# Performance work log

Measured on AMD Instinct MI355X. Metric: run time of the kernel, lower is better.

Reference implementation:

```python
import jax, jax.numpy as jnp
import numpy as np

B = 1024           # number of drug pairs (graphs per side)
ATOMS = 64         # atoms per molecule
N = B * ATOMS      # total atoms per side
H = 512            # hidden_size * number_of_molecules
FFN_H = 2048
OUT = 86           # num_tasks


def setup_inputs() -> dict:
    key = jax.random.key(0)
    ks = jax.random.split(key, 12)
    inv = 1.0 / np.sqrt(H)
    inv2 = 1.0 / np.sqrt(2 * H)
    invf = 1.0 / np.sqrt(FFN_H)
    return {
        "left_output": jax.random.normal(ks[0], (B, H), jnp.float32),
        "right_output": jax.random.normal(ks[1], (B, H), jnp.float32),
        "left_atom": jax.random.normal(ks[2], (N, H), jnp.float32),
        "right_atom": jax.random.normal(ks[3], (N, H), jnp.float32),
        "left_batch": jnp.arange(N, dtype=jnp.int32) // ATOMS,
        "right_batch": jnp.arange(N, dtype=jnp.int32) // ATOMS,
        "noise": jax.random.uniform(ks[4], (B, H), jnp.float32),
        "w_i_w": jax.random.normal(ks[5], (H, H), jnp.float32) * inv,
        "w_i_b": jnp.zeros((H,), jnp.float32),
        "prj_i_w": jax.random.normal(ks[6], (H, H), jnp.float32) * inv,
        "prj_i_b": jnp.zeros((H,), jnp.float32),
        "ffn1_w": jax.random.normal(ks[7], (2 * H, FFN_H), jnp.float32) * inv2,
        "ffn1_b": jnp.zeros((FFN_H,), jnp.float32),
        "ffn2_w": jax.random.normal(ks[8], (FFN_H, OUT), jnp.float32) * invf,
        "ffn2_b": jnp.zeros((OUT,), jnp.float32),
    }


def _seg_softmax(s, seg, num_segments):
    m = jax.ops.segment_max(s, seg, num_segments=num_segments)
    e = jnp.exp(s - m[seg])
    z = jax.ops.segment_sum(e, seg, num_segments=num_segments)
    return e / z[seg]


def reference(left_output, right_output, left_atom, right_atom,
              left_batch, right_batch, noise,
              w_i_w, w_i_b, prj_i_w, prj_i_b,
              ffn1_w, ffn1_b, ffn2_w, ffn2_b):
    # repeat_interleave(left_output, degree(right_batch)) == gather by segment id
    left_align = left_output[right_batch]    # [N_r, H]
    right_align = right_output[left_batch]   # [N_l, H]

    # cross-molecule coattention scores (elementwise product + reduce)
    left_scores = jnp.sum((left_atom @ w_i_w + w_i_b) * (right_align @ prj_i_w + prj_i_b), axis=-1)
    left_scores = _seg_softmax(left_scores, left_batch, B)
    right_scores = jnp.sum((right_atom @ w_i_w + w_i_b) * (left_align @ prj_i_w + prj_i_b), axis=-1)
    right_scores = _seg_softmax(right_scores, right_batch, B)

    # attention-weighted global add pool
    h_output = jax.ops.segment_sum(left_atom * right_align * left_scores[:, None], left_batch, num_segments=B)
    t_output = jax.ops.segment_sum(right_atom * left_align * right_scores[:, None], right_batch, num_segments=B)

    # sign-directed noise perturbation (same noise for both sides, as in original)
    nrm = jnp.maximum(jnp.linalg.norm(noise, axis=-1, keepdims=True), 1e-12)
    noise_n = noise / nrm
    h_pert = h_output + jnp.sign(h_output) * noise_n * 0.1
    t_pert = t_output + jnp.sign(t_output) * noise_n * 0.1

    pair = jnp.concatenate([h_pert, t_pert], axis=-1)  # [B, 2H]
    hid = jax.nn.relu(pair @ ffn1_w + ffn1_b)
    output = hid @ ffn2_w + ffn2_b  # training mode: raw logits, no sigmoid
    return (output, h_output, h_pert, left_scores, right_scores, left_output, right_output)
```

## Files before the change

kernel.cpp:

```cpp
#include <hip/hip_runtime.h>
#include <hip/hip_bf16.h>
#include <float.h>

#define B_ 1024
#define H_ 512
#define N_ (B_ * 64)
#define FFN_ 2048
#define OUT_ 86

typedef __bf16 bf16_t;
typedef __attribute__((ext_vector_type(8))) __bf16 bf16x8;
typedef __attribute__((ext_vector_type(4))) float f32x4;

__device__ __forceinline__ float wred_sum(float v) {
#pragma unroll
  for (int m = 32; m; m >>= 1) v += __shfl_xor(v, m);
  return v;
}
__device__ __forceinline__ float wred_max(float v) {
#pragma unroll
  for (int m = 32; m; m >>= 1) v = fmaxf(v, __shfl_xor(v, m));
  return v;
}

__device__ __forceinline__ void gload_lds16(const void* g, void* l) {
  __builtin_amdgcn_global_load_lds((const __attribute__((address_space(1))) unsigned int*)g,
                                   (__attribute__((address_space(3))) unsigned int*)l, 16, 0, 0);
}

template <bool BT, bool BIAS>
__global__ __launch_bounds__(256) void gemm64(const float* __restrict__ A1, const float* __restrict__ A2,
                                              int M1, const float* __restrict__ Bm,
                                              const float* __restrict__ bias, float* __restrict__ C,
                                              int N, int K) {
  __shared__ float As[16][68];
  __shared__ float Bs[16][68];
  const int bm = blockIdx.x * 64, bn = blockIdx.y * 64;
  const float* __restrict__ A = (bm < M1) ? (A1 + (size_t)bm * K) : (A2 + (size_t)(bm - M1) * K);
  const int t = threadIdx.x;
  const int tx = t & 15, ty = t >> 4;
  float acc[4][4] = {};
  for (int k0 = 0; k0 < K; k0 += 16) {
#pragma unroll
    for (int i = 0; i < 4; i++) {
      int m = (t >> 4) + i * 16;
      As[t & 15][m] = A[(size_t)m * K + k0 + (t & 15)];
    }
    if (BT) {
#pragma unroll
      for (int i = 0; i < 4; i++) {
        int n = (t >> 4) + i * 16;
        Bs[t & 15][n] = Bm[(size_t)(bn + n) * K + k0 + (t & 15)];
      }
    } else {
#pragma unroll
      for (int i = 0; i < 4; i++) {
        int kk = (t >> 6) + i * 4;
        Bs[kk][t & 63] = Bm[(size_t)(k0 + kk) * N + bn + (t & 63)];
      }
    }
    __syncthreads();
#pragma unroll
    for (int kk = 0; kk < 16; kk++) {
      float4 av = *(const float4*)&As[kk][ty * 4];
      float4 bv = *(const float4*)&Bs[kk][tx * 4];
      float a_[4] = {av.x, av.y, av.z, av.w};
      float b_[4] = {bv.x, bv.y, bv.z, bv.w};
#pragma unroll
      for (int i = 0; i < 4; i++)
#pragma unroll
        for (int j = 0; j < 4; j++) acc[i][j] += a_[i] * b_[j];
    }
    __syncthreads();
  }
#pragma unroll
  for (int i = 0; i < 4; i++) {
    int m = bm + ty * 4 + i;
    float tmp[4];
#pragma unroll
    for (int j = 0; j < 4; j++) {
      float x = acc[i][j];
      if (BIAS) x += bias[bn + tx * 4 + j];
      tmp[j] = x;
    }
    float4 v;
    v.x = tmp[0]; v.y = tmp[1]; v.z = tmp[2]; v.w = tmp[3];
    *(float4*)&C[(size_t)m * N + bn + tx * 4] = v;
  }
}

__global__ __launch_bounds__(512, 4) void k_atoms11(const float* __restrict__ atomL, const float* __restrict__ atomR,
                                                    const float* __restrict__ uLR,
                                                    float* __restrict__ scoresL, float* __restrict__ scoresR,
                                                    float* __restrict__ pL, float* __restrict__ pR) {
  const int pair = blockIdx.x;
  const int side = pair >> 10, b = pair & 1023;
  const int t = threadIdx.x, wave = t >> 6, lane = t & 63;

  __shared__ float s_all[64];
  __shared__ float s_nrm[64];
  __shared__ float pp[8][512];

  const float* __restrict__ atom = side ? atomR : atomL;
  const float* __restrict__ u = uLR + (size_t)pair * H_;
  f32x4 u0 = *(const f32x4*)&u[lane * 4];
  f32x4 u1 = *(const f32x4*)&u[256 + lane * 4];

  const float* __restrict__ base = atom + ((size_t)b * 64 + wave * 8) * H_ + lane * 4;

  f32x4 A0[8], A1[8];
#pragma unroll
  for (int i = 0; i < 8; i++) {
    const float* r0 = base + (size_t)i * H_;
    asm volatile("global_load_dwordx4 %0, %1, off" : "=&v"(A0[i]) : "v"(r0) : "memory");
    asm volatile("global_load_dwordx4 %0, %1, off" : "=&v"(A1[i]) : "v"(r0 + 256) : "memory");
  }

  float d[8];
#pragma unroll
  for (int i = 0; i < 8; i++) {
    switch (14 - 2 * i) {
      case 14: asm volatile("s_waitcnt vmcnt(14)" ::: "memory"); break;
      case 12: asm volatile("s_waitcnt vmcnt(12)" ::: "memory"); break;
      case 10: asm volatile("s_waitcnt vmcnt(10)" ::: "memory"); break;
      case 8:  asm volatile("s_waitcnt vmcnt(8)"  ::: "memory"); break;
      case 6:  asm volatile("s_waitcnt vmcnt(6)"  ::: "memory"); break;
      case 4:  asm volatile("s_waitcnt vmcnt(4)"  ::: "memory"); break;
      case 2:  asm volatile("s_waitcnt vmcnt(2)"  ::: "memory"); break;
      default: asm volatile("s_waitcnt vmcnt(0)"  ::: "memory"); break;
    }
    __builtin_amdgcn_sched_barrier(0);
    d[i] = A0[i].x * u0.x + A0[i].y * u0.y + A0[i].z * u0.z + A0[i].w * u0.w +
           A1[i].x * u1.x + A1[i].y * u1.y + A1[i].z * u1.z + A1[i].w * u1.w;
  }

#pragma unroll
  for (int i = 0; i < 8; i++) d[i] = wred_sum(d[i]);
  if (lane < 8) {
    float myv = 0.f;
#pragma unroll
    for (int i = 0; i < 8; i++) myv = (lane == i) ? d[i] : myv;
    s_all[wave * 8 + lane] = myv;
  }
  __syncthreads();
  {
    float sv = s_all[lane];
    float M = wred_max(sv);
    float e = __expf(sv - M);
    float Z = wred_sum(e);
    float w_n = e / Z;
    if (wave == 0) {
      s_nrm[lane] = w_n;
      (side ? scoresR : scoresL)[(size_t)b * 64 + lane] = w_n;
    }
  }
  __syncthreads();

  f32x4 q0 = {0.f, 0.f, 0.f, 0.f}, q1 = {0.f, 0.f, 0.f, 0.f};
#pragma unroll
  for (int i = 0; i < 8; i++) {
    const float w = s_nrm[wave * 8 + i];
    q0.x += w * A0[i].x; q0.y += w * A0[i].y; q0.z += w * A0[i].z; q0.w += w * A0[i].w;
    q1.x += w * A1[i].x; q1.y += w * A1[i].y; q1.z += w * A1[i].z; q1.w += w * A1[i].w;
  }
  *(f32x4*)&pp[wave][lane * 4] = q0;
  *(f32x4*)&pp[wave][256 + lane * 4] = q1;
  __syncthreads();

  float v = pp[0][t] + pp[1][t] + pp[2][t] + pp[3][t] +
            pp[4][t] + pp[5][t] + pp[6][t] + pp[7][t];
  (side ? pR : pL)[(size_t)b * H_ + t] = v;
}

__global__ __launch_bounds__(512) void k_pert(const float* __restrict__ lo, const float* __restrict__ ro,
                                              const float* __restrict__ noise,
                                              const float* __restrict__ pL, const float* __restrict__ pR,
                                              float* __restrict__ h_out, float* __restrict__ h_pert,
                                              bf16_t* __restrict__ pairbf) {
  const int b = blockIdx.x, t = threadIdx.x;
  float nv = noise[(size_t)b * H_ + t];
  float sq = nv * nv;
  sq = wred_sum(sq);
  __shared__ float red[8];
  if ((t & 63) == 0) red[t >> 6] = sq;
  __syncthreads();
  float tot = 0.f;
#pragma unroll
  for (int i = 0; i < 8; i++) tot += red[i];
  float nrm = fmaxf(sqrtf(tot), 1e-12f);
  float nn = nv / nrm * 0.1f;
  float h = ro[(size_t)b * H_ + t] * pL[(size_t)b * H_ + t];
  float tt = lo[(size_t)b * H_ + t] * pR[(size_t)b * H_ + t];
  float sh = (h > 0.f) ? 1.f : ((h < 0.f) ? -1.f : 0.f);
  float st = (tt > 0.f) ? 1.f : ((tt < 0.f) ? -1.f : 0.f);
  float hp = h + sh * nn;
  float tp = tt + st * nn;
  h_out[(size_t)b * H_ + t] = h;
  h_pert[(size_t)b * H_ + t] = hp;
  pairbf[(size_t)b * 1024 + t] = (bf16_t)hp;
  pairbf[(size_t)b * 1024 + 512 + t] = (bf16_t)tp;
}

__global__ __launch_bounds__(256) void k_w1t(const float* __restrict__ W1, bf16_t* __restrict__ W1t) {
  __shared__ float tile[32][33];
  const int bx = blockIdx.x;
  const int by = blockIdx.y;
  const int tx = threadIdx.x & 31, ty = threadIdx.x >> 5;
#pragma unroll
  for (int i = ty; i < 32; i += 8)
    tile[i][tx] = W1[(size_t)(by * 32 + i) * FFN_ + bx * 32 + tx];
  __syncthreads();
#pragma unroll
  for (int i = ty; i < 32; i += 8)
    W1t[(size_t)(bx * 32 + i) * 1024 + by * 32 + tx] = (bf16_t)tile[tx][i];
}

__global__ __launch_bounds__(256) void k_ffn1(const bf16_t* __restrict__ Abf, const bf16_t* __restrict__ Bt,
                                              const float* __restrict__ bias, float* __restrict__ C) {
  __shared__ bf16_t As[64 * 64];
  __shared__ bf16_t Bs[64 * 64];
  const int bm = blockIdx.x * 64, bn = blockIdx.y * 64;
  const int t = threadIdx.x;
  const int lane = t & 63, wave = t >> 6;
  const int wm = wave & 1, wn = wave >> 1;
  const int l15 = lane & 15, l4 = lane >> 4;
  f32x4 acc[2][2] = {{{0.f, 0.f, 0.f, 0.f}, {0.f, 0.f, 0.f, 0.f}},
                     {{0.f, 0.f, 0.f, 0.f}, {0.f, 0.f, 0.f, 0.f}}};

  for (int k0 = 0; k0 < 1024; k0 += 64) {
#pragma unroll
    for (int r = 0; r < 2; r++) {
      const int off = (r * 256 + t) * 16;
      const int row = off >> 7;
      const int g = (off >> 4) & 7;
      const int scb = ((g ^ (row & 7)) << 4);
      gload_lds16((const char*)Abf + (size_t)(bm + row) * 2048 + k0 * 2 + scb, (char*)As + off);
      gload_lds16((const char*)Bt + (size_t)(bn + row) * 2048 + k0 * 2 + scb, (char*)Bs + off);
    }
    __syncthreads();
#pragma unroll
    for (int ks = 0; ks < 2; ks++) {
      const int ar0 = wm * 32 + l15, ar1 = ar0 + 16;
      const int br0 = wn * 32 + l15, br1 = br0 + 16;
      const int gA = ks * 4 + l4;
      bf16x8 a0 = *(const bf16x8*)((const char*)As + ar0 * 128 + ((gA ^ (ar0 & 7)) << 4));
      bf16x8 a1 = *(const bf16x8*)((const char*)As + ar1 * 128 + ((gA ^ (ar1 & 7)) << 4));
      bf16x8 b0 = *(const bf16x8*)((const char*)Bs + br0 * 128 + ((gA ^ (br0 & 7)) << 4));
      bf16x8 b1 = *(const bf16x8*)((const char*)Bs + br1 * 128 + ((gA ^ (br1 & 7)) << 4));
      acc[0][0] = __builtin_amdgcn_mfma_f32_16x16x32_bf16(a0, b0, acc[0][0], 0, 0, 0);
      acc[0][1] = __builtin_amdgcn_mfma_f32_16x16x32_bf16(a0, b1, acc[0][1], 0, 0, 0);
      acc[1][0] = __builtin_amdgcn_mfma_f32_16x16x32_bf16(a1, b0, acc[1][0], 0, 0, 0);
      acc[1][1] = __builtin_amdgcn_mfma_f32_16x16x32_bf16(a1, b1, acc[1][1], 0, 0, 0);
    }
    __syncthreads();
  }
#pragma unroll
  for (int mi = 0; mi < 2; mi++)
#pragma unroll
    for (int nj = 0; nj < 2; nj++)
#pragma unroll
      for (int r = 0; r < 4; r++) {
        const int m = bm + wm * 32 + mi * 16 + l4 * 4 + r;
        const int n = bn + wn * 32 + nj * 16 + l15;
        float v = acc[mi][nj][r] + bias[n];
        C[(size_t)m * FFN_ + n] = fmaxf(v, 0.f);
      }
}

__global__ void k_w2t(const float* __restrict__ W2, float* __restrict__ W2t) {
  int idx = blockIdx.x * 256 + threadIdx.x;
  if (idx < OUT_ * FFN_) {
    int n = idx / FFN_, k = idx % FFN_;
    W2t[idx] = W2[(size_t)k * OUT_ + n];
  }
}

__global__ __launch_bounds__(256) void k_ffn2(const float* __restrict__ hid, const float* __restrict__ W2t,
                                              const float* __restrict__ b2, float* __restrict__ out) {
  const int b0 = blockIdx.x * 2;
  const int t = threadIdx.x, wave = t >> 6, lane = t & 63;
  float4 h0[8], h1[8];
  const float* r0 = hid + (size_t)b0 * FFN_;
#pragma unroll
  for (int j = 0; j < 8; j++) {
    h0[j] = *(const float4*)&r0[lane * 4 + j * 256];
    h1[j] = *(const float4*)&r0[FFN_ + lane * 4 + j * 256];
  }
  for (int n = wave; n < OUT_; n += 4) {
    const float* wrow = W2t + (size_t)n * FFN_;
    float s0 = 0.f, s1 = 0.f;
#pragma unroll
    for (int j = 0; j < 8; j++) {
      float4 w4 = *(const float4*)&wrow[lane * 4 + j * 256];
      s0 += w4.x * h0[j].x + w4.y * h0[j].y + w4.z * h0[j].z + w4.w * h0[j].w;
      s1 += w4.x * h1[j].x + w4.y * h1[j].y + w4.z * h1[j].z + w4.w * h1[j].w;
    }
    s0 = wred_sum(s0);
    s1 = wred_sum(s1);
    if (lane == 0) {
      out[(size_t)b0 * OUT_ + n] = s0 + b2[n];
      out[(size_t)(b0 + 1) * OUT_ + n] = s1 + b2[n];
    }
  }
}

extern "C" void kernel_launch(void* const* d_in, const int* in_sizes, int n_in,
                              void* d_out, int out_size, void* d_ws, size_t ws_size,
                              hipStream_t stream) {
  const float* lo = (const float*)d_in[0];
  const float* ro = (const float*)d_in[1];
  const float* la = (const float*)d_in[2];
  const float* ra = (const float*)d_in[3];
  const float* noise = (const float*)d_in[6];
  const float* w_i_w = (const float*)d_in[7];
  const float* prj_w = (const float*)d_in[9];
  const float* prj_b = (const float*)d_in[10];
  const float* W1 = (const float*)d_in[11];
  const float* b1 = (const float*)d_in[12];
  const float* W2 = (const float*)d_in[13];
  const float* b2 = (const float*)d_in[14];

  float* out = (float*)d_out;
  float* o_logits = out;
  float* o_hout  = out + 88064;
  float* o_hpert = o_hout + 524288;
  float* o_ls    = o_hpert + 524288;
  float* o_rs    = o_ls + 65536;
  float* o_lo    = o_rs + 65536;
  float* o_ro    = o_lo + 524288;

  float* ws = (float*)d_ws;
  float* T    = ws; ws += 2048 * 512;
  float* uLR  = ws; ws += 2048 * 512;
  float* pL   = ws; ws += B_ * H_;
  float* pR   = ws; ws += B_ * H_;
  float* hid  = ws; ws += B_ * FFN_;
  float* W2t  = ws; ws += OUT_ * FFN_;
  bf16_t* pairbf = (bf16_t*)ws; ws += B_ * 1024 / 2;
  bf16_t* W1t    = (bf16_t*)ws; ws += FFN_ * 1024 / 2;

  gemm64<false, true><<<dim3(32, 8), 256, 0, stream>>>(ro, lo, 1024, prj_w, prj_b, T, 512, 512);
  gemm64<true, false><<<dim3(32, 8), 256, 0, stream>>>(T, T, 1 << 30, w_i_w, nullptr, uLR, 512, 512);
  k_w1t<<<dim3(64, 32), 256, 0, stream>>>(W1, W1t);
  k_atoms11<<<2048, 512, 0, stream>>>(la, ra, uLR, o_ls, o_rs, pL, pR);
  k_pert<<<1024, 512, 0, stream>>>(lo, ro, noise, pL, pR, o_hout, o_hpert, pairbf);
  k_ffn1<<<dim3(16, 32), 256, 0, stream>>>(pairbf, W1t, b1, hid);
  k_w2t<<<688, 256, 0, stream>>>(W2, W2t);
  k_ffn2<<<512, 256, 0, stream>>>(hid, W2t, b2, o_logits);
  hipMemcpyAsync(o_lo, lo, (size_t)B_ * H_ * 4, hipMemcpyDeviceToDevice, stream);
  hipMemcpyAsync(o_ro, ro, (size_t)B_ * H_ * 4, hipMemcpyDeviceToDevice, stream);
}
```

Baseline: 161.7 us.

## Fuse atom attention pooling with noise perturbation into one 1024-thread kernel

Merges the per-side atom pooling kernel and the perturbation kernel into one kernel where each block handles both sides of a pair (16 waves). The pooled pL/pR vectors stay in shared memory instead of a global round trip, and one launch is removed. In exchange, blocks grow to 1024 threads with 32KB of shared pooling buffers, which may lower occupancy, and the noise norm reduction is merged into the same barrier sequence.

```diff
diff --git a/kernel.cpp b/kernel.cpp
--- a/kernel.cpp
+++ b/kernel.cpp
@@ -89,24 +89,29 @@
   }
 }
 
-__global__ __launch_bounds__(512, 4) void k_atoms11(const float* __restrict__ atomL, const float* __restrict__ atomR,
+__global__ __launch_bounds__(1024, 4) void k_atomsF(const float* __restrict__ atomL, const float* __restrict__ atomR,
                                                     const float* __restrict__ uLR,
+                                                    const float* __restrict__ lo, const float* __restrict__ ro,
+                                                    const float* __restrict__ noise,
                                                     float* __restrict__ scoresL, float* __restrict__ scoresR,
-                                                    float* __restrict__ pL, float* __restrict__ pR) {
-  const int pair = blockIdx.x;
-  const int side = pair >> 10, b = pair & 1023;
+                                                    float* __restrict__ h_out, float* __restrict__ h_pert,
+                                                    bf16_t* __restrict__ pairbf) {
+  const int b = blockIdx.x;
   const int t = threadIdx.x, wave = t >> 6, lane = t & 63;
-
-  __shared__ float s_all[64];
-  __shared__ float s_nrm[64];
-  __shared__ float pp[8][512];
+  const int side = wave >> 3;
+  const int w8 = wave & 7;
+
+  __shared__ float s_all[2][64];
+  __shared__ float s_nrm[2][64];
+  __shared__ float pp[16][512];
+  __shared__ float red[16];
 
   const float* __restrict__ atom = side ? atomR : atomL;
-  const float* __restrict__ u = uLR + (size_t)pair * H_;
+  const float* __restrict__ u = uLR + ((size_t)side * 1024 + b) * H_;
   f32x4 u0 = *(const f32x4*)&u[lane * 4];
   f32x4 u1 = *(const f32x4*)&u[256 + lane * 4];
 
-  const float* __restrict__ base = atom + ((size_t)b * 64 + wave * 8) * H_ + lane * 4;
+  const float* __restrict__ base = atom + ((size_t)b * 64 + w8 * 8) * H_ + lane * 4;
 
   f32x4 A0[8], A1[8];
 #pragma unroll
@@ -140,65 +145,57 @@
     float myv = 0.f;
 #pragma unroll
     for (int i = 0; i < 8; i++) myv = (lane == i) ? d[i] : myv;
-    s_all[wave * 8 + lane] = myv;
+    s_all[side][w8 * 8 + lane] = myv;
   }
   __syncthreads();
   {
-    float sv = s_all[lane];
+    float sv = s_all[side][lane];
     float M = wred_max(sv);
     float e = __expf(sv - M);
     float Z = wred_sum(e);
     float w_n = e / Z;
-    if (wave == 0) {
-      s_nrm[lane] = w_n;
-      (side ? scoresR : scoresL)[(size_t)b * 64 + lane] = w_n;
-    }
+    if (wave == 0) { s_nrm[0][lane] = w_n; scoresL[(size_t)b * 64 + lane] = w_n; }
+    if (wave == 8) { s_nrm[1][lane] = w_n; scoresR[(size_t)b * 64 + lane] = w_n; }
   }
   __syncthreads();
 
   f32x4 q0 = {0.f, 0.f, 0.f, 0.f}, q1 = {0.f, 0.f, 0.f, 0.f};
 #pragma unroll
   for (int i = 0; i < 8; i++) {
-    const float w = s_nrm[wave * 8 + i];
+    const float w = s_nrm[side][w8 * 8 + i];
     q0.x += w * A0[i].x; q0.y += w * A0[i].y; q0.z += w * A0[i].z; q0.w += w * A0[i].w;
     q1.x += w * A1[i].x; q1.y += w * A1[i].y; q1.z += w * A1[i].z; q1.w += w * A1[i].w;
   }
   *(f32x4*)&pp[wave][lane * 4] = q0;
   *(f32x4*)&pp[wave][256 + lane * 4] = q1;
-  __syncthreads();
-
-  float v = pp[0][t] + pp[1][t] + pp[2][t] + pp[3][t] +
-            pp[4][t] + pp[5][t] + pp[6][t] + pp[7][t];
-  (side ? pR : pL)[(size_t)b * H_ + t] = v;
-}
-
-__global__ __launch_bounds__(512) void k_pert(const float* __restrict__ lo, const float* __restrict__ ro,
-                                              const float* __restrict__ noise,
-                                              const float* __restrict__ pL, const float* __restrict__ pR,
-                                              float* __restrict__ h_out, float* __restrict__ h_pert,
-                                              bf16_t* __restrict__ pairbf) {
-  const int b = blockIdx.x, t = threadIdx.x;
-  float nv = noise[(size_t)b * H_ + t];
-  float sq = nv * nv;
+
+  float nv = 0.f, sq = 0.f;
+  if (t < 512) { nv = noise[(size_t)b * H_ + t]; sq = nv * nv; }
   sq = wred_sum(sq);
-  __shared__ float red[8];
-  if ((t & 63) == 0) red[t >> 6] = sq;
+  if (lane == 0) red[wave] = sq;
   __syncthreads();
   float tot = 0.f;
 #pragma unroll
-  for (int i = 0; i < 8; i++) tot += red[i];
-  float nrm = fmaxf(sqrtf(tot), 1e-12f);
-  float nn = nv / nrm * 0.1f;
-  float h = ro[(size_t)b * H_ + t] * pL[(size_t)b * H_ + t];
-  float tt = lo[(size_t)b * H_ + t] * pR[(size_t)b * H_ + t];
-  float sh = (h > 0.f) ? 1.f : ((h < 0.f) ? -1.f : 0.f);
-  float st = (tt > 0.f) ? 1.f : ((tt < 0.f) ? -1.f : 0.f);
-  float hp = h + sh * nn;
-  float tp = tt + st * nn;
-  h_out[(size_t)b * H_ + t] = h;
-  h_pert[(size_t)b * H_ + t] = hp;
-  pairbf[(size_t)b * 1024 + t] = (bf16_t)hp;
-  pairbf[(size_t)b * 1024 + 512 + t] = (bf16_t)tp;
+  for (int i = 0; i < 16; i++) tot += red[i];
+  const float rn = 0.1f / fmaxf(sqrtf(tot), 1e-12f);
+
+  if (t < 512) {
+    float pLv = pp[0][t] + pp[1][t] + pp[2][t] + pp[3][t] +
+                pp[4][t] + pp[5][t] + pp[6][t] + pp[7][t];
+    float pRv = pp[8][t] + pp[9][t] + pp[10][t] + pp[11][t] +
+                pp[12][t] + pp[13][t] + pp[14][t] + pp[15][t];
+    float nn = nv * rn;
+    float h = ro[(size_t)b * H_ + t] * pLv;
+    float tt = lo[(size_t)b * H_ + t] * pRv;
+    float sh = (h > 0.f) ? 1.f : ((h < 0.f) ? -1.f : 0.f);
+    float st = (tt > 0.f) ? 1.f : ((tt < 0.f) ? -1.f : 0.f);
+    float hp = h + sh * nn;
+    float tp = tt + st * nn;
+    h_out[(size_t)b * H_ + t] = h;
+    h_pert[(size_t)b * H_ + t] = hp;
+    pairbf[(size_t)b * 1024 + t] = (bf16_t)hp;
+    pairbf[(size_t)b * 1024 + 512 + t] = (bf16_t)tp;
+  }
 }
 
 __global__ __launch_bounds__(256) void k_w1t(const float* __restrict__ W1, bf16_t* __restrict__ W1t) {
@@ -332,8 +329,6 @@
   float* ws = (float*)d_ws;
   float* T    = ws; ws += 2048 * 512;
   float* uLR  = ws; ws += 2048 * 512;
-  float* pL   = ws; ws += B_ * H_;
-  float* pR   = ws; ws += B_ * H_;
   float* hid  = ws; ws += B_ * FFN_;
   float* W2t  = ws; ws += OUT_ * FFN_;
   bf16_t* pairbf = (bf16_t*)ws; ws += B_ * 1024 / 2;
@@ -342,8 +337,7 @@
   gemm64<false, true><<<dim3(32, 8), 256, 0, stream>>>(ro, lo, 1024, prj_w, prj_b, T, 512, 512);
   gemm64<true, false><<<dim3(32, 8), 256, 0, stream>>>(T, T, 1 << 30, w_i_w, nullptr, uLR, 512, 512);
   k_w1t<<<dim3(64, 32), 256, 0, stream>>>(W1, W1t);
-  k_atoms11<<<2048, 512, 0, stream>>>(la, ra, uLR, o_ls, o_rs, pL, pR);
-  k_pert<<<1024, 512, 0, stream>>>(lo, ro, noise, pL, pR, o_hout, o_hpert, pairbf);
+  k_atomsF<<<1024, 1024, 0, stream>>>(la, ra, uLR, lo, ro, noise, o_ls, o_rs, o_hout, o_hpert, pairbf);
   k_ffn1<<<dim3(16, 32), 256, 0, stream>>>(pairbf, W1t, b1, hid);
   k_w2t<<<688, 256, 0, stream>>>(W2, W2t);
   k_ffn2<<<512, 256, 0, stream>>>(hid, W2t, b2, o_logits);
```

Measured after the change: 165.9 us. +2.6%, slower.

## Fuse per-pair atom attention for both sides with noise perturbation kernel

Applied to the files above, without the earlier changes.

Merges the left/right atom-attention kernel and the perturbation kernel into one block per graph pair that loads both sides' atom rows at once. The pooled vectors stay in registers instead of round-tripping through workspace buffers, and one kernel launch is removed. The trade-off is half as many blocks, double the register footprint per thread (launch bounds lowered to 2 blocks per SIMD), and less parallelism for a memory-bound stream over 268 MB of atoms.

```diff
diff --git a/kernel.cpp b/kernel.cpp
--- a/kernel.cpp
+++ b/kernel.cpp
@@ -89,108 +89,136 @@
   }
 }
 
-__global__ __launch_bounds__(512, 4) void k_atoms11(const float* __restrict__ atomL, const float* __restrict__ atomR,
-                                                    const float* __restrict__ uLR,
-                                                    float* __restrict__ scoresL, float* __restrict__ scoresR,
-                                                    float* __restrict__ pL, float* __restrict__ pR) {
-  const int pair = blockIdx.x;
-  const int side = pair >> 10, b = pair & 1023;
+__global__ __launch_bounds__(512, 2) void k_atomsP(const float* __restrict__ atomL, const float* __restrict__ atomR,
+                                                   const float* __restrict__ uLR,
+                                                   const float* __restrict__ lo, const float* __restrict__ ro,
+                                                   const float* __restrict__ noise,
+                                                   float* __restrict__ scoresL, float* __restrict__ scoresR,
+                                                   float* __restrict__ h_out, float* __restrict__ h_pert,
+                                                   bf16_t* __restrict__ pairbf) {
+  const int b = blockIdx.x;
   const int t = threadIdx.x, wave = t >> 6, lane = t & 63;
 
   __shared__ float s_all[64];
   __shared__ float s_nrm[64];
   __shared__ float pp[8][512];
-
-  const float* __restrict__ atom = side ? atomR : atomL;
-  const float* __restrict__ u = uLR + (size_t)pair * H_;
-  f32x4 u0 = *(const f32x4*)&u[lane * 4];
-  f32x4 u1 = *(const f32x4*)&u[256 + lane * 4];
-
-  const float* __restrict__ base = atom + ((size_t)b * 64 + wave * 8) * H_ + lane * 4;
-
-  f32x4 A0[8], A1[8];
+  __shared__ float red[8];
+
+  const float* __restrict__ uL = uLR + (size_t)b * H_;
+  const float* __restrict__ uR = uLR + ((size_t)1024 + b) * H_;
+  f32x4 uL0 = *(const f32x4*)&uL[lane * 4];
+  f32x4 uL1 = *(const f32x4*)&uL[256 + lane * 4];
+  f32x4 uR0 = *(const f32x4*)&uR[lane * 4];
+  f32x4 uR1 = *(const f32x4*)&uR[256 + lane * 4];
+
+  const float* __restrict__ baseL = atomL + ((size_t)b * 64 + wave * 8) * H_ + lane * 4;
+  const float* __restrict__ baseR = atomR + ((size_t)b * 64 + wave * 8) * H_ + lane * 4;
+
+  f32x4 A0[8], A1[8], B0[8], B1[8];
 #pragma unroll
   for (int i = 0; i < 8; i++) {
-    const float* r0 = base + (size_t)i * H_;
+    const float* r0 = baseL + (size_t)i * H_;
     asm volatile("global_load_dwordx4 %0, %1, off" : "=&v"(A0[i]) : "v"(r0) : "memory");
     asm volatile("global_load_dwordx4 %0, %1, off" : "=&v"(A1[i]) : "v"(r0 + 256) : "memory");
   }
-
-  float d[8];
 #pragma unroll
   for (int i = 0; i < 8; i++) {
-    switch (14 - 2 * i) {
-      case 14: asm volatile("s_waitcnt vmcnt(14)" ::: "memory"); break;
-      case 12: asm volatile("s_waitcnt vmcnt(12)" ::: "memory"); break;
-      case 10: asm volatile("s_waitcnt vmcnt(10)" ::: "memory"); break;
-      case 8:  asm volatile("s_waitcnt vmcnt(8)"  ::: "memory"); break;
-      case 6:  asm volatile("s_waitcnt vmcnt(6)"  ::: "memory"); break;
-      case 4:  asm volatile("s_waitcnt vmcnt(4)"  ::: "memory"); break;
-      case 2:  asm volatile("s_waitcnt vmcnt(2)"  ::: "memory"); break;
-      default: asm volatile("s_waitcnt vmcnt(0)"  ::: "memory"); break;
-    }
-    __builtin_amdgcn_sched_barrier(0);
-    d[i] = A0[i].x * u0.x + A0[i].y * u0.y + A0[i].z * u0.z + A0[i].w * u0.w +
-           A1[i].x * u1.x + A1[i].y * u1.y + A1[i].z * u1.z + A1[i].w * u1.w;
-  }
-
-#pragma unroll
-  for (int i = 0; i < 8; i++) d[i] = wred_sum(d[i]);
-  if (lane < 8) {
-    float myv = 0.f;
-#pragma unroll
-    for (int i = 0; i < 8; i++) myv = (lane == i) ? d[i] : myv;
-    s_all[wave * 8 + lane] = myv;
-  }
-  __syncthreads();
+    const float* r0 = baseR + (size_t)i * H_;
+    asm volatile("global_load_dwordx4 %0, %1, off" : "=&v"(B0[i]) : "v"(r0) : "memory");
+    asm volatile("global_load_dwordx4 %0, %1, off" : "=&v"(B1[i]) : "v"(r0 + 256) : "memory");
+  }
+
+  float pLv, pRv;
+
+  asm volatile("s_waitcnt vmcnt(16)" ::: "memory");
+  __builtin_amdgcn_sched_barrier(0);
   {
+    float d[8];
+#pragma unroll
+    for (int i = 0; i < 8; i++)
+      d[i] = A0[i].x * uL0.x + A0[i].y * uL0.y + A0[i].z * uL0.z + A0[i].w * uL0.w +
+             A1[i].x * uL1.x + A1[i].y * uL1.y + A1[i].z * uL1.z + A1[i].w * uL1.w;
+#pragma unroll
+    for (int i = 0; i < 8; i++) d[i] = wred_sum(d[i]);
+    if (lane < 8) {
+      float myv = 0.f;
+#pragma unroll
+      for (int i = 0; i < 8; i++) myv = (lane == i) ? d[i] : myv;
+      s_all[wave * 8 + lane] = myv;
+    }
+    __syncthreads();
     float sv = s_all[lane];
     float M = wred_max(sv);
     float e = __expf(sv - M);
     float Z = wred_sum(e);
     float w_n = e / Z;
-    if (wave == 0) {
-      s_nrm[lane] = w_n;
-      (side ? scoresR : scoresL)[(size_t)b * 64 + lane] = w_n;
-    }
-  }
-  __syncthreads();
-
-  f32x4 q0 = {0.f, 0.f, 0.f, 0.f}, q1 = {0.f, 0.f, 0.f, 0.f};
-#pragma unroll
-  for (int i = 0; i < 8; i++) {
-    const float w = s_nrm[wave * 8 + i];
-    q0.x += w * A0[i].x; q0.y += w * A0[i].y; q0.z += w * A0[i].z; q0.w += w * A0[i].w;
-    q1.x += w * A1[i].x; q1.y += w * A1[i].y; q1.z += w * A1[i].z; q1.w += w * A1[i].w;
-  }
-  *(f32x4*)&pp[wave][lane * 4] = q0;
-  *(f32x4*)&pp[wave][256 + lane * 4] = q1;
-  __syncthreads();
-
-  float v = pp[0][t] + pp[1][t] + pp[2][t] + pp[3][t] +
-            pp[4][t] + pp[5][t] + pp[6][t] + pp[7][t];
-  (side ? pR : pL)[(size_t)b * H_ + t] = v;
-}
-
-__global__ __launch_bounds__(512) void k_pert(const float* __restrict__ lo, const float* __restrict__ ro,
-                                              const float* __restrict__ noise,
-                                              const float* __restrict__ pL, const float* __restrict__ pR,
-                                              float* __restrict__ h_out, float* __restrict__ h_pert,
-                                              bf16_t* __restrict__ pairbf) {
-  const int b = blockIdx.x, t = threadIdx.x;
+    if (wave == 0) { s_nrm[lane] = w_n; scoresL[(size_t)b * 64 + lane] = w_n; }
+    __syncthreads();
+    f32x4 q0 = {0.f, 0.f, 0.f, 0.f}, q1 = {0.f, 0.f, 0.f, 0.f};
+#pragma unroll
+    for (int i = 0; i < 8; i++) {
+      const float w = s_nrm[wave * 8 + i];
+      q0.x += w * A0[i].x; q0.y += w * A0[i].y; q0.z += w * A0[i].z; q0.w += w * A0[i].w;
+      q1.x += w * A1[i].x; q1.y += w * A1[i].y; q1.z += w * A1[i].z; q1.w += w * A1[i].w;
+    }
+    *(f32x4*)&pp[wave][lane * 4] = q0;
+    *(f32x4*)&pp[wave][256 + lane * 4] = q1;
+    __syncthreads();
+    pLv = pp[0][t] + pp[1][t] + pp[2][t] + pp[3][t] +
+          pp[4][t] + pp[5][t] + pp[6][t] + pp[7][t];
+    __syncthreads();
+  }
+
+  asm volatile("s_waitcnt vmcnt(0)" ::: "memory");
+  __builtin_amdgcn_sched_barrier(0);
+  {
+    float d[8];
+#pragma unroll
+    for (int i = 0; i < 8; i++)
+      d[i] = B0[i].x * uR0.x + B0[i].y * uR0.y + B0[i].z * uR0.z + B0[i].w * uR0.w +
+             B1[i].x * uR1.x + B1[i].y * uR1.y + B1[i].z * uR1.z + B1[i].w * uR1.w;
+#pragma unroll
+    for (int i = 0; i < 8; i++) d[i] = wred_sum(d[i]);
+    if (lane < 8) {
+      float myv = 0.f;
+#pragma unroll
+      for (int i = 0; i < 8; i++) myv = (lane == i) ? d[i] : myv;
+      s_all[wave * 8 + lane] = myv;
+    }
+    __syncthreads();
+    float sv = s_all[lane];
+    float M = wred_max(sv);
+    float e = __expf(sv - M);
+    float Z = wred_sum(e);
+    float w_n = e / Z;
+    if (wave == 0) { s_nrm[lane] = w_n; scoresR[(size_t)b * 64 + lane] = w_n; }
+    __syncthreads();
+    f32x4 q0 = {0.f, 0.f, 0.f, 0.f}, q1 = {0.f, 0.f, 0.f, 0.f};
+#pragma unroll
+    for (int i = 0; i < 8; i++) {
+      const float w = s_nrm[wave * 8 + i];
+      q0.x += w * B0[i].x; q0.y += w * B0[i].y; q0.z += w * B0[i].z; q0.w += w * B0[i].w;
+      q1.x += w * B1[i].x; q1.y += w * B1[i].y; q1.z += w * B1[i].z; q1.w += w * B1[i].w;
+    }
+    *(f32x4*)&pp[wave][lane * 4] = q0;
+    *(f32x4*)&pp[wave][256 + lane * 4] = q1;
+    __syncthreads();
+    pRv = pp[0][t] + pp[1][t] + pp[2][t] + pp[3][t] +
+          pp[4][t] + pp[5][t] + pp[6][t] + pp[7][t];
+  }
+
   float nv = noise[(size_t)b * H_ + t];
-  float sq = nv * nv;
-  sq = wred_sum(sq);
-  __shared__ float red[8];
-  if ((t & 63) == 0) red[t >> 6] = sq;
+  float sq = wred_sum(nv * nv);
+  if (lane == 0) red[wave] = sq;
   __syncthreads();
   float tot = 0.f;
 #pragma unroll
   for (int i = 0; i < 8; i++) tot += red[i];
-  float nrm = fmaxf(sqrtf(tot), 1e-12f);
-  float nn = nv / nrm * 0.1f;
-  float h = ro[(size_t)b * H_ + t] * pL[(size_t)b * H_ + t];
-  float tt = lo[(size_t)b * H_ + t] * pR[(size_t)b * H_ + t];
+  const float rn = 0.1f / fmaxf(sqrtf(tot), 1e-12f);
+
+  float nn = nv * rn;
+  float h = ro[(size_t)b * H_ + t] * pLv;
+  float tt = lo[(size_t)b * H_ + t] * pRv;
   float sh = (h > 0.f) ? 1.f : ((h < 0.f) ? -1.f : 0.f);
   float st = (tt > 0.f) ? 1.f : ((tt < 0.f) ? -1.f : 0.f);
   float hp = h + sh * nn;
@@ -332,8 +360,6 @@
   float* ws = (float*)d_ws;
   float* T    = ws; ws += 2048 * 512;
   float* uLR  = ws; ws += 2048 * 512;
-  float* pL   = ws; ws += B_ * H_;
-  float* pR   = ws; ws += B_ * H_;
   float* hid  = ws; ws += B_ * FFN_;
   float* W2t  = ws; ws += OUT_ * FFN_;
   bf16_t* pairbf = (bf16_t*)ws; ws += B_ * 1024 / 2;
@@ -342,8 +368,7 @@
   gemm64<false, true><<<dim3(32, 8), 256, 0, stream>>>(ro, lo, 1024, prj_w, prj_b, T, 512, 512);
   gemm64<true, false><<<dim3(32, 8), 256, 0, stream>>>(T, T, 1 << 30, w_i_w, nullptr, uLR, 512, 512);
   k_w1t<<<dim3(64, 32), 256, 0, stream>>>(W1, W1t);
-  k_atoms11<<<2048, 512, 0, stream>>>(la, ra, uLR, o_ls, o_rs, pL, pR);
-  k_pert<<<1024, 512, 0, stream>>>(lo, ro, noise, pL, pR, o_hout, o_hpert, pairbf);
+  k_atomsP<<<1024, 512, 0, stream>>>(la, ra, uLR, lo, ro, noise, o_ls, o_rs, o_hout, o_hpert, pairbf);
   k_ffn1<<<dim3(16, 32), 256, 0, stream>>>(pairbf, W1t, b1, hid);
   k_w2t<<<688, 256, 0, stream>>>(W2, W2t);
   k_ffn2<<<512, 256, 0, stream>>>(hid, W2t, b2, o_logits);
```

Result: slower. 171.8 us (+6.3%).
